# Kernel optimization log

Measured on AMD Instinct MI355X. Metric: run time of the kernel, lower is better.

## Reference

```python
import jax, jax.numpy as jnp
import numpy as np

B, S, E, H, NL = 64, 256, 1024, 16, 2
D = E // H          # head dim = 64
FF = 4 * E          # 4096
EPS = 1e-5
MASKED = -10000.0   # masked_bias buffer value


def layer_norm(x, g, b):
    m = jnp.mean(x, axis=-1, keepdims=True)
    v = jnp.mean(jnp.square(x - m), axis=-1, keepdims=True)
    return (x - m) * jax.lax.rsqrt(v + EPS) * g + b


def setup_inputs() -> dict:
    key = jax.random.key(0)
    ks = jax.random.split(key, 8)
    s = 0.02
    return {
        "sentence_hidden": jax.random.normal(ks[0], (B, S, E), dtype=jnp.float32),
        "wpe": jax.random.normal(ks[1], (256, E), dtype=jnp.float32) * s,
        "ln1_g": jnp.ones((NL, E), jnp.float32),
        "ln1_b": jnp.zeros((NL, E), jnp.float32),
        "attn_w": jax.random.normal(ks[2], (NL, E, 3 * E), dtype=jnp.float32) * s,
        "attn_b": jnp.zeros((NL, 3 * E), jnp.float32),
        "attn_proj_w": jax.random.normal(ks[3], (NL, E, E), dtype=jnp.float32) * s,
        "attn_proj_b": jnp.zeros((NL, E), jnp.float32),
        "ln2_g": jnp.ones((NL, E), jnp.float32),
        "ln2_b": jnp.zeros((NL, E), jnp.float32),
        "fc_w": jax.random.normal(ks[4], (NL, E, FF), dtype=jnp.float32) * s,
        "fc_b": jnp.zeros((NL, FF), jnp.float32),
        "mlp_proj_w": jax.random.normal(ks[5], (NL, FF, E), dtype=jnp.float32) * s,
        "mlp_proj_b": jnp.zeros((NL, E), jnp.float32),
        "lnf_g": jnp.ones((E,), jnp.float32),
        "lnf_b": jnp.zeros((E,), jnp.float32),
    }


def reference(sentence_hidden, wpe, ln1_g, ln1_b, attn_w, attn_b, attn_proj_w,
              attn_proj_b, ln2_g, ln2_b, fc_w, fc_b, mlp_proj_w, mlp_proj_b,
              lnf_g, lnf_b):
    # position embeddings: positions 0..S-1 (wpe has 256 rows, S == 256)
    h = sentence_hidden + wpe[:S][None, :, :]
    causal = jnp.tril(jnp.ones((S, S), dtype=bool))  # [S,S]
    scale = 1.0 / np.sqrt(D)
    for i in range(NL):
        # --- attention ---
        x = layer_norm(h, ln1_g[i], ln1_b[i])
        qkv = x @ attn_w[i] + attn_b[i]                    # [B,S,3E]
        q, k, v = jnp.split(qkv, 3, axis=-1)
        q = q.reshape(B, S, H, D).transpose(0, 2, 1, 3)    # [B,H,S,D]
        k = k.reshape(B, S, H, D).transpose(0, 2, 1, 3)
        v = v.reshape(B, S, H, D).transpose(0, 2, 1, 3)
        w = jnp.einsum("bhqd,bhkd->bhqk", q, k) * scale    # [B,H,S,S]
        w = jnp.where(causal, w, jnp.asarray(MASKED, w.dtype))
        w = jax.nn.softmax(w, axis=-1)
        a = jnp.einsum("bhqk,bhkd->bhqd", w, v)            # [B,H,S,D]
        a = a.transpose(0, 2, 1, 3).reshape(B, S, E)
        a = a @ attn_proj_w[i] + attn_proj_b[i]
        h = h + a
        # --- MLP ---
        x = layer_norm(h, ln2_g[i], ln2_b[i])
        m = jax.nn.gelu(x @ fc_w[i] + fc_b[i], approximate=True)  # gelu_new
        m = m @ mlp_proj_w[i] + mlp_proj_b[i]
        h = h + m
    h = layer_norm(h, lnf_g, lnf_b)
    loss = jnp.mean(jnp.square(h[0, :-1, :] - sentence_hidden[0, 1:, :]))
    return (h, loss)
```

## Files before the change

kernel.cpp:

```cpp
#include <hip/hip_runtime.h>
#include <cstdint>
#include <cstddef>


typedef __attribute__((ext_vector_type(4))) float f32x4;
typedef __attribute__((ext_vector_type(16))) float f32x16;
typedef __attribute__((ext_vector_type(8))) __bf16 bf16x8;
typedef __attribute__((ext_vector_type(4))) unsigned int u32x4;
typedef __attribute__((ext_vector_type(8))) unsigned short u16x8;
typedef __attribute__((ext_vector_type(4))) unsigned short u16x4;

__device__ __forceinline__ unsigned short f2bf(float x) {
  unsigned int u = __builtin_bit_cast(unsigned int, x);
  u += 0x7fffu + ((u >> 16) & 1u);
  return (unsigned short)(u >> 16);
}
__device__ __forceinline__ float gelu_new(float x) {
  float u = 0.7978845608028654f * (x + 0.044715f * x * x * x);
  return x * __builtin_amdgcn_rcpf(1.0f + __expf(-2.0f * u));
}
__device__ __forceinline__ unsigned int cvtpk(float lo, float hi) {
  unsigned int r;
  asm("v_cvt_pk_bf16_f32 %0, %1, %2" : "=v"(r) : "v"(lo), "v"(hi));
  return r;
}
__device__ __forceinline__ void plswap(unsigned int& a, unsigned int& b) {
  asm("v_permlane32_swap_b32 %0, %1" : "+v"(a), "+v"(b));
}

__global__ __launch_bounds__(256) void transpose_bf16(
    const float* __restrict__ W, unsigned short* __restrict__ Wt, int K, int N) {
  __shared__ float tile[32][33];
  const int n0 = blockIdx.x * 32, k0 = blockIdx.y * 32;
  const int tx = threadIdx.x, ty = threadIdx.y;
#pragma unroll
  for (int j = 0; j < 32; j += 8)
    tile[ty + j][tx] = W[(size_t)(k0 + ty + j) * N + n0 + tx];
  __syncthreads();
#pragma unroll
  for (int j = 0; j < 32; j += 8)
    Wt[(size_t)(n0 + ty + j) * K + k0 + tx] = f2bf(tile[tx][ty + j]);
}

__device__ __forceinline__ void ln_core(
    f32x4 v, const float* g, const float* bb, int row, int t,
    int outf32, void* outp) {
  float s = v.x + v.y + v.z + v.w;
  float sq = v.x * v.x + v.y * v.y + v.z * v.z + v.w * v.w;
#pragma unroll
  for (int off = 32; off; off >>= 1) {
    s += __shfl_xor(s, off, 64);
    sq += __shfl_xor(sq, off, 64);
  }
  __shared__ float red[8];
  if ((t & 63) == 0) { red[t >> 6] = s; red[4 + (t >> 6)] = sq; }
  __syncthreads();
  s = red[0] + red[1] + red[2] + red[3];
  sq = red[4] + red[5] + red[6] + red[7];
  const float mean = s * (1.0f / 1024.0f);
  const float var = sq * (1.0f / 1024.0f) - mean * mean;
  const float rs = rsqrtf(var + 1e-5f);
  const f32x4 gv = ((const f32x4*)g)[t];
  const f32x4 bv = ((const f32x4*)bb)[t];
  float y0 = (v.x - mean) * rs * gv.x + bv.x;
  float y1 = (v.y - mean) * rs * gv.y + bv.y;
  float y2 = (v.z - mean) * rs * gv.z + bv.z;
  float y3 = (v.w - mean) * rs * gv.w + bv.w;
  if (outf32) {
    f32x4 o; o.x = y0; o.y = y1; o.z = y2; o.w = y3;
    ((f32x4*)outp)[(size_t)row * 256 + t] = o;
  } else {
    u16x4 pk;
    pk.x = f2bf(y0); pk.y = f2bf(y1); pk.z = f2bf(y2); pk.w = f2bf(y3);
    ((u16x4*)outp)[(size_t)row * 256 + t] = pk;
  }
}

template <int OUTF32>
__global__ __launch_bounds__(256) void ln_kernel(
    const float* __restrict__ hin, const float* __restrict__ g,
    const float* __restrict__ bb, void* __restrict__ outp) {
  const int row = blockIdx.x, t = threadIdx.x;
  const f32x4 v = ((const f32x4*)(hin + (size_t)row * 1024))[t];
  ln_core(v, g, bb, row, t, OUTF32, outp);
}

__global__ __launch_bounds__(256) void ln_wpe_kernel(
    const float* __restrict__ sent, const float* __restrict__ wpe,
    const float* __restrict__ g, const float* __restrict__ bb,
    float* __restrict__ h, unsigned short* __restrict__ xb) {
  const int row = blockIdx.x, t = threadIdx.x;
  const int s = row & 255;
  f32x4 a = ((const f32x4*)(sent + (size_t)row * 1024))[t];
  f32x4 w = ((const f32x4*)(wpe + (size_t)s * 1024))[t];
  f32x4 v = a + w;
  ((f32x4*)(h + (size_t)row * 1024))[t] = v;
  ln_core(v, g, bb, row, t, 0, xb);
}

template <int BM, int EPI>
__global__ __launch_bounds__(512, 2) void gemm8p(
    const unsigned short* __restrict__ A, const unsigned short* __restrict__ Bt,
    const float* __restrict__ bias, unsigned short* __restrict__ Cb,
    float* __restrict__ Hres, int N, int K, int gx, int gy) {
  constexpr int M_REP = BM / 32;
  constexpr int MH = M_REP / 2;
  constexpr int A_E = BM * 64;
  constexpr int BUF_E = A_E + 16384;
  __shared__ alignas(16) unsigned short smem[2 * BUF_E];

  const int nwg = gx * gy;
  const int dd = blockIdx.x;
  const int wrk = (dd & 7) * (nwg >> 3) + (dd >> 3);
  const int stripe = gy * 4;
  const int cg = wrk / stripe;
  const int rem = wrk - cg * stripe;
  const int by = rem >> 2;
  const int bx = cg * 4 + (rem & 3);
  const int row0 = by * BM, col0 = bx * 256;

  const int t = threadIdx.x;
  const int wid = t >> 6, l = t & 63;
  const int wm = wid >> 2, wn = wid & 3;
  const int fr = l & 15, q4 = l >> 4;

  const int cx0 = (q4 ^ (fr & 7)) * 8;
  const int cx1 = ((4 + q4) ^ (fr & 7)) * 8;
  const int b_r0 = (wn * 64 + fr) * 64;
  auto a_slot = [&](int m) -> int {
    if constexpr (BM == 256) return (wm * 128 + m * 16 + fr) * 64;
    else return ((m >> 1) * 64 + wm * 32 + (m & 1) * 16 + fr) * 64;
  };

  const int lrow = l >> 3;
  const int scol = ((l & 7) ^ (lrow & 7)) * 8;

  auto stB = [&](int tt, int win) {
    const unsigned short* s =
        Bt + (size_t)(col0 + win * 8 + lrow) * K + tt * 64 + scol;
    __builtin_amdgcn_global_load_lds(
        (const __attribute__((address_space(1))) void*)s,
        (__attribute__((address_space(3))) void*)(smem + (tt & 1) * BUF_E + A_E + win * 512),
        16, 0, 0);
  };
  auto stA = [&](int tt, int win) {
    int rb;
    if constexpr (BM == 256) rb = win * 8;
    else rb = ((win >> 2) & 1) * 64 + (win >> 3) * 32 + (win & 3) * 8;
    const unsigned short* s =
        A + (size_t)(row0 + rb + lrow) * K + tt * 64 + scol;
    __builtin_amdgcn_global_load_lds(
        (const __attribute__((address_space(1))) void*)s,
        (__attribute__((address_space(3))) void*)(smem + (tt & 1) * BUF_E + win * 512),
        16, 0, 0);
  };
  auto stageB_set = [&](int tt) {
    stB(tt, 2 * wid); stB(tt, 2 * wid + 1);
    stB(tt, 16 + 2 * wid); stB(tt, 16 + 2 * wid + 1);
  };
  auto stageA_set = [&](int tt) {
    if constexpr (BM == 256) {
      const int i0 = 2 * wid, i1 = 2 * wid + 1;
      stA(tt, i0 < 8 ? i0 : 8 + i0);
      stA(tt, i1 < 8 ? i1 : 8 + i1);
      stA(tt, i0 < 8 ? 8 + i0 : 16 + i0);
      stA(tt, i1 < 8 ? 8 + i1 : 16 + i1);
    } else {
      stA(tt, wid);
      stA(tt, 8 + wid);
    }
  };
  constexpr int VM_BOUND = (BM == 256) ? 2 : 1;

  const int nt = K >> 6;

  stageB_set(0);
  stageA_set(0);
  asm volatile("s_waitcnt vmcnt(%0)" :: "i"(VM_BOUND) : "memory");
  __builtin_amdgcn_s_barrier();
  asm volatile("" ::: "memory");

  f32x4 acc[M_REP][4];
#pragma unroll
  for (int m = 0; m < M_REP; ++m)
#pragma unroll
    for (int n = 0; n < 4; ++n) {
      acc[m][n].x = 0.f; acc[m][n].y = 0.f; acc[m][n].z = 0.f; acc[m][n].w = 0.f;
    }

  for (int tc = 0; tc < nt; ++tc) {
    const unsigned short* Ab = smem + (tc & 1) * BUF_E;
    const unsigned short* Bb = Ab + A_E;
    const bool pf = (tc + 1) < nt;

    bf16x8 bfr[4][2], af[MH][2];
#pragma unroll
    for (int n = 0; n < 4; ++n) {
      bfr[n][0] = *(const bf16x8*)(Bb + b_r0 + n * 1024 + cx0);
      bfr[n][1] = *(const bf16x8*)(Bb + b_r0 + n * 1024 + cx1);
    }
#pragma unroll
    for (int m = 0; m < MH; ++m) {
      af[m][0] = *(const bf16x8*)(Ab + a_slot(m) + cx0);
      af[m][1] = *(const bf16x8*)(Ab + a_slot(m) + cx1);
    }
    if (pf) stageB_set(tc + 1);
    __builtin_amdgcn_s_setprio(1);
#pragma unroll
    for (int m = 0; m < MH; ++m)
#pragma unroll
      for (int n = 0; n < 4; ++n) {
        acc[m][n] = __builtin_amdgcn_mfma_f32_16x16x32_bf16(
            af[m][0], bfr[n][0], acc[m][n], 0, 0, 0);
        acc[m][n] = __builtin_amdgcn_mfma_f32_16x16x32_bf16(
            af[m][1], bfr[n][1], acc[m][n], 0, 0, 0);
      }
    __builtin_amdgcn_s_setprio(0);
    if (pf) asm volatile("s_waitcnt vmcnt(4)" ::: "memory");
    else    asm volatile("s_waitcnt vmcnt(0)" ::: "memory");
    __builtin_amdgcn_s_barrier();
    asm volatile("" ::: "memory");

    bf16x8 ah[MH][2];
#pragma unroll
    for (int m = 0; m < MH; ++m) {
      ah[m][0] = *(const bf16x8*)(Ab + a_slot(MH + m) + cx0);
      ah[m][1] = *(const bf16x8*)(Ab + a_slot(MH + m) + cx1);
    }
    if (pf) stageA_set(tc + 1);
    __builtin_amdgcn_s_setprio(1);
#pragma unroll
    for (int m = 0; m < MH; ++m)
#pragma unroll
      for (int n = 0; n < 4; ++n) {
        acc[MH + m][n] = __builtin_amdgcn_mfma_f32_16x16x32_bf16(
            ah[m][0], bfr[n][0], acc[MH + m][n], 0, 0, 0);
        acc[MH + m][n] = __builtin_amdgcn_mfma_f32_16x16x32_bf16(
            ah[m][1], bfr[n][1], acc[MH + m][n], 0, 0, 0);
      }
    __builtin_amdgcn_s_setprio(0);
    if (pf) asm volatile("s_waitcnt vmcnt(%0)" :: "i"(VM_BOUND) : "memory");
    else    asm volatile("s_waitcnt vmcnt(0)" ::: "memory");
    __builtin_amdgcn_s_barrier();
    asm volatile("" ::: "memory");
  }

  if constexpr (EPI == 2) {
#pragma unroll
    for (int n = 0; n < 4; ++n) {
      const int col = col0 + wn * 64 + n * 16 + fr;
      const float bi = bias[col];
#pragma unroll
      for (int m = 0; m < M_REP; ++m)
#pragma unroll
        for (int e = 0; e < 4; ++e) {
          const int row = row0 + wm * (BM / 2) + m * 16 + q4 * 4 + e;
          Hres[(size_t)row * N + col] += acc[m][n][e] + bi;
        }
    }
  } else {
    char* wreg = (char*)smem + wid * 9216;
    float bi[4];
#pragma unroll
    for (int n = 0; n < 4; ++n) bi[n] = bias[col0 + wn * 64 + n * 16 + fr];
#pragma unroll
    for (int half = 0; half < M_REP / 4; ++half) {
#pragma unroll
      for (int m = 0; m < 4; ++m)
#pragma unroll
        for (int n = 0; n < 4; ++n)
#pragma unroll
          for (int e = 0; e < 4; ++e) {
            float v = acc[half * 4 + m][n][e] + bi[n];
            if (EPI == 1) v = gelu_new(v);
            *(unsigned short*)(wreg + (m * 16 + q4 * 4 + e) * 144 +
                               (n * 16 + fr) * 2) = f2bf(v);
          }
#pragma unroll
      for (int rb = 0; rb < 8; ++rb) {
        const int rowl = rb * 8 + (l >> 3);
        u16x8 vv = *(const u16x8*)(wreg + rowl * 144 + (l & 7) * 16);
        const int rg = row0 + wm * (BM / 2) + half * 64 + rowl;
        *(u16x8*)(Cb + (size_t)rg * N + col0 + wn * 64 + (l & 7) * 8) = vv;
      }
    }
  }
}

__global__ __launch_bounds__(256) void attn_mfma(
    const unsigned short* __restrict__ qkv, unsigned short* __restrict__ aout,
    int b0) {
  __shared__ alignas(16) unsigned short Klds[256 * 64];
  __shared__ alignas(16) unsigned short Vt[64 * 256];
  const int bh = blockIdx.x;
  const int bl = bh >> 4, hd = bh & 15;
  const size_t base = (size_t)bl * 256 * 3072 + (size_t)hd * 64;
  const int t = threadIdx.x;
  const int w = t >> 6, l = t & 63;
  const int lq = l & 31, hl = l >> 5;

#pragma unroll
  for (int i = 0; i < 8; ++i) {
    const int r = i * 32 + (t >> 3);
    const int c = t & 7;
    u16x8 kv = *(const u16x8*)(qkv + base + (size_t)r * 3072 + 1024 + c * 8);
    *(u16x8*)(Klds + r * 64 + ((c ^ (r & 7)) * 8)) = kv;
    u16x8 vv = *(const u16x8*)(qkv + base + (size_t)r * 3072 + 2048 + c * 8);
#pragma unroll
    for (int j = 0; j < 8; ++j) {
      const int d = c * 8 + j;
      Vt[d * 256 + (((r >> 3) ^ (d & 31)) * 8) + (r & 7)] = vv[j];
    }
  }

  const int q0 = w * 64;
  bf16x8 qf[2][4];
#pragma unroll
  for (int n = 0; n < 2; ++n)
#pragma unroll
    for (int d16 = 0; d16 < 4; ++d16)
      qf[n][d16] = *(const bf16x8*)(qkv + base +
          (size_t)(q0 + n * 32 + lq) * 3072 + d16 * 16 + hl * 8);
  __syncthreads();

  const float cs = 0.125f * 1.44269504088896f;
  f32x16 O[2][2];
#pragma unroll
  for (int m = 0; m < 2; ++m)
#pragma unroll
    for (int n = 0; n < 2; ++n)
#pragma unroll
      for (int e = 0; e < 16; ++e) O[m][n][e] = 0.f;
  float mrun[2] = {-3.0e38f, -3.0e38f};
  float lrun[2] = {0.f, 0.f};

  const int ktmax = (q0 + 63) >> 5;
  for (int kt = 0; kt <= ktmax; ++kt) {
    bf16x8 kf[4];
    const int krow = kt * 32 + lq;
#pragma unroll
    for (int d16 = 0; d16 < 4; ++d16) {
      const int chunk = (d16 * 2 + hl) ^ (krow & 7);
      kf[d16] = *(const bf16x8*)(Klds + krow * 64 + chunk * 8);
    }
    const int nlo = (kt * 32 > q0 + 31) ? 1 : 0;
    bf16x8 pfrag[2][2];
#pragma unroll
    for (int n = 0; n < 2; ++n) {
      if (n < nlo) continue;
      f32x16 s;
#pragma unroll
      for (int e = 0; e < 16; ++e) s[e] = 0.f;
#pragma unroll
      for (int d16 = 0; d16 < 4; ++d16)
        s = __builtin_amdgcn_mfma_f32_32x32x16_bf16(kf[d16], qf[n][d16], s, 0, 0, 0);
      const int qg = q0 + n * 32 + lq;
      float sv[16];
#pragma unroll
      for (int r = 0; r < 16; ++r) {
        const int kg = kt * 32 + (r & 3) + 8 * (r >> 2) + 4 * hl;
        const float x = s[r] * cs;
        sv[r] = (kg > qg) ? -3.0e38f : x;
      }
      float pmax = sv[0];
#pragma unroll
      for (int r = 1; r < 16; ++r) pmax = fmaxf(pmax, sv[r]);
      pmax = fmaxf(pmax, __shfl_xor(pmax, 32, 64));
      const float nm = fmaxf(mrun[n], pmax);
      const float alpha = exp2f(mrun[n] - nm);
      mrun[n] = nm;
      float psum = 0.f;
#pragma unroll
      for (int r = 0; r < 16; ++r) {
        sv[r] = exp2f(sv[r] - nm);
        psum += sv[r];
      }
      psum += __shfl_xor(psum, 32, 64);
      lrun[n] = lrun[n] * alpha + psum;
#pragma unroll
      for (int m = 0; m < 2; ++m)
#pragma unroll
        for (int e = 0; e < 16; ++e) O[m][n][e] *= alpha;
#pragma unroll
      for (int h = 0; h < 2; ++h) {
        unsigned int a0 = cvtpk(sv[h * 8 + 0], sv[h * 8 + 1]);
        unsigned int a1 = cvtpk(sv[h * 8 + 2], sv[h * 8 + 3]);
        unsigned int c0 = cvtpk(sv[h * 8 + 4], sv[h * 8 + 5]);
        unsigned int c1 = cvtpk(sv[h * 8 + 6], sv[h * 8 + 7]);
        plswap(a0, c0);
        plswap(a1, c1);
        u32x4 fw; fw.x = a0; fw.y = a1; fw.z = c0; fw.w = c1;
        pfrag[n][h] = __builtin_bit_cast(bf16x8, fw);
      }
    }
#pragma unroll
    for (int m = 0; m < 2; ++m)
#pragma unroll
      for (int h = 0; h < 2; ++h) {
        const int dd = m * 32 + lq;
        const int chunk = (kt * 4 + h * 2 + hl) ^ (dd & 31);
        bf16x8 vf = *(const bf16x8*)(Vt + dd * 256 + chunk * 8);
#pragma unroll
        for (int n = 0; n < 2; ++n)
          if (n >= nlo)
            O[m][n] = __builtin_amdgcn_mfma_f32_32x32x16_bf16(vf, pfrag[n][h], O[m][n], 0, 0, 0);
      }
  }

#pragma unroll
  for (int n = 0; n < 2; ++n) {
    const float inv = 1.0f / lrun[n];
    const size_t row = (size_t)(b0 + bl) * 256 + q0 + n * 32 + lq;
#pragma unroll
    for (int m = 0; m < 2; ++m) {
#pragma unroll
      for (int qd = 0; qd < 4; ++qd) {
        u16x4 pk;
#pragma unroll
        for (int e = 0; e < 4; ++e) pk[e] = f2bf(O[m][n][qd * 4 + e] * inv);
        *(u16x4*)(aout + row * 1024 + hd * 64 + m * 32 + qd * 8 + hl * 4) = pk;
      }
    }
  }
}

__device__ __forceinline__ float block_reduce_sum256(float v) {
#pragma unroll
  for (int off = 32; off; off >>= 1) v += __shfl_xor(v, off, 64);
  __shared__ float red[4];
  const int t = threadIdx.x;
  if ((t & 63) == 0) red[t >> 6] = v;
  __syncthreads();
  return red[0] + red[1] + red[2] + red[3];
}

__global__ __launch_bounds__(256) void loss_partial(
    const float* __restrict__ hf, const float* __restrict__ sent,
    float* __restrict__ part) {
  const int s = blockIdx.x, t = threadIdx.x;
  f32x4 a = ((const f32x4*)(hf + (size_t)s * 1024))[t];
  f32x4 b = ((const f32x4*)(sent + (size_t)(s + 1) * 1024))[t];
  f32x4 d = a - b;
  float v = d.x * d.x + d.y * d.y + d.z * d.z + d.w * d.w;
  float tot = block_reduce_sum256(v);
  if (t == 0) part[s] = tot;
}

__global__ __launch_bounds__(256) void loss_final(
    const float* __restrict__ part, float* __restrict__ out) {
  const int t = threadIdx.x;
  float v = (t < 255) ? part[t] : 0.f;
  float s = block_reduce_sum256(v);
  if (t == 0) out[0] = s * (1.0f / (255.0f * 1024.0f));
}

constexpr size_t OFF_X     = 0;
constexpr size_t OFF_QKV   = 33554432;
constexpr size_t OFF_WQKV  = OFF_QKV + 67108864;
constexpr size_t OFF_WPROJ = OFF_WQKV + 6291456;
constexpr size_t OFF_WFC   = OFF_WPROJ + 2097152;
constexpr size_t OFF_WMLP  = OFF_WFC + 8388608;
constexpr size_t OFF_PART  = OFF_WMLP + 8388608;

extern "C" void kernel_launch(void* const* d_in, const int* in_sizes, int n_in,
                              void* d_out, int out_size, void* d_ws, size_t ws_size,
                              hipStream_t stream) {
  (void)in_sizes; (void)n_in; (void)out_size; (void)ws_size;
  const float* sent    = (const float*)d_in[0];
  const float* wpe     = (const float*)d_in[1];
  const float* ln1_g   = (const float*)d_in[2];
  const float* ln1_b   = (const float*)d_in[3];
  const float* attn_w  = (const float*)d_in[4];
  const float* attn_b  = (const float*)d_in[5];
  const float* attn_pw = (const float*)d_in[6];
  const float* attn_pb = (const float*)d_in[7];
  const float* ln2_g   = (const float*)d_in[8];
  const float* ln2_b   = (const float*)d_in[9];
  const float* fc_w    = (const float*)d_in[10];
  const float* fc_b    = (const float*)d_in[11];
  const float* mlp_w   = (const float*)d_in[12];
  const float* mlp_b   = (const float*)d_in[13];
  const float* lnf_g   = (const float*)d_in[14];
  const float* lnf_b   = (const float*)d_in[15];
  float* out_h = (float*)d_out;

  char* ws = (char*)d_ws;
  float* h              = out_h;
  unsigned short* xb    = (unsigned short*)(ws + OFF_X);
  unsigned short* qkvb  = (unsigned short*)(ws + OFF_QKV);
  unsigned short* mb    = (unsigned short*)(ws + OFF_QKV);
  unsigned short* wqkv  = (unsigned short*)(ws + OFF_WQKV);
  unsigned short* wproj = (unsigned short*)(ws + OFF_WPROJ);
  unsigned short* wfc   = (unsigned short*)(ws + OFF_WFC);
  unsigned short* wmlp  = (unsigned short*)(ws + OFF_WMLP);
  float* part           = (float*)(ws + OFF_PART);

  const dim3 tb(32, 8, 1);
  for (int i = 0; i < 2; ++i) {
    transpose_bf16<<<dim3(96, 32), tb, 0, stream>>>(
        attn_w + (size_t)i * 1024 * 3072, wqkv, 1024, 3072);
    transpose_bf16<<<dim3(32, 32), tb, 0, stream>>>(
        attn_pw + (size_t)i * 1024 * 1024, wproj, 1024, 1024);
    transpose_bf16<<<dim3(128, 32), tb, 0, stream>>>(
        fc_w + (size_t)i * 1024 * 4096, wfc, 1024, 4096);
    transpose_bf16<<<dim3(32, 128), tb, 0, stream>>>(
        mlp_w + (size_t)i * 4096 * 1024, wmlp, 4096, 1024);

    if (i == 0)
      ln_wpe_kernel<<<16384, 256, 0, stream>>>(sent, wpe, ln1_g, ln1_b, h, xb);
    else
      ln_kernel<0><<<16384, 256, 0, stream>>>(h, ln1_g + i * 1024, ln1_b + i * 1024, xb);
    for (int c = 0; c < 2; ++c) {
      const size_t r0 = (size_t)c * 8192;
      gemm8p<256, 0><<<384, 512, 0, stream>>>(
          xb + r0 * 1024, wqkv, attn_b + i * 3072, qkvb, nullptr, 3072, 1024, 12, 32);
      attn_mfma<<<512, 256, 0, stream>>>(qkvb, xb, c * 32);
    }
    gemm8p<256, 2><<<256, 512, 0, stream>>>(
        xb, wproj, attn_pb + i * 1024, nullptr, h, 1024, 1024, 4, 64);

    ln_kernel<0><<<16384, 256, 0, stream>>>(h, ln2_g + i * 1024, ln2_b + i * 1024, xb);
    for (int c = 0; c < 2; ++c) {
      const size_t r0 = (size_t)c * 8192;
      gemm8p<256, 1><<<512, 512, 0, stream>>>(
          xb + r0 * 1024, wfc, fc_b + i * 4096, mb, nullptr, 4096, 1024, 16, 32);
      gemm8p<128, 2><<<256, 512, 0, stream>>>(
          mb, wmlp, mlp_b + i * 1024, nullptr, h + r0 * 1024, 1024, 4096, 4, 64);
    }
  }

  ln_kernel<1><<<16384, 256, 0, stream>>>(h, lnf_g, lnf_b, out_h);
  loss_partial<<<255, 256, 0, stream>>>(out_h, sent, part);
  loss_final<<<1, 256, 0, stream>>>(part, out_h + 16777216);
}
```

Measured before the change: 1.257 ms.

## Add 4-phase 256x256 GEMM and process all rows at once when workspace allows

Adds a new gemm4p kernel that splits each K-step into four half-tile MFMA phases. Loads for the next tile are staged into LDS between phases, and MFMA sections run at raised wave priority. When the workspace is large enough, the QKV, attention and FC/MLP GEMMs run over the full 16384 rows in one launch instead of two 8192-row chunks, which raises the grid size and cuts launches. The path depends on ws_size, and the finer barrier scheduling could add sync overhead.

```diff
diff --git a/kernel.cpp b/kernel.cpp
--- a/kernel.cpp
+++ b/kernel.cpp
@@ -98,6 +98,197 @@
   ln_core(v, g, bb, row, t, 0, xb);
 }
 
+template <int EPI>
+__global__ __launch_bounds__(512, 2) void gemm4p(
+    const unsigned short* __restrict__ A, const unsigned short* __restrict__ Bt,
+    const float* __restrict__ bias, unsigned short* __restrict__ Cb,
+    float* __restrict__ Hres, int N, int K, int gx, int gy) {
+  constexpr int A_E = 16384;
+  constexpr int BUF_E = A_E + 16384;
+  __shared__ alignas(16) unsigned short smem[2 * BUF_E];
+
+  const int nwg = gx * gy;
+  const int dd = blockIdx.x;
+  const int wrk = (dd & 7) * (nwg >> 3) + (dd >> 3);
+  const int stripe = gy * 4;
+  const int cg = wrk / stripe;
+  const int rem = wrk - cg * stripe;
+  const int by = rem >> 2;
+  const int bx = cg * 4 + (rem & 3);
+  const int row0 = by * 256, col0 = bx * 256;
+
+  const int t = threadIdx.x;
+  const int wid = t >> 6, l = t & 63;
+  const int wm = wid >> 2, wn = wid & 3;
+  const int fr = l & 15, q4 = l >> 4;
+
+  const int cx0 = (q4 ^ (fr & 7)) * 8;
+  const int cx1 = ((4 + q4) ^ (fr & 7)) * 8;
+  const int b_r0 = (wn * 64 + fr) * 64;
+  auto a_slot = [&](int m) -> int { return (wm * 128 + m * 16 + fr) * 64; };
+
+  const int lrow = l >> 3;
+  const int scol = ((l & 7) ^ (lrow & 7)) * 8;
+
+  auto stB = [&](int tt, int win) {
+    const unsigned short* s =
+        Bt + (size_t)(col0 + win * 8 + lrow) * K + tt * 64 + scol;
+    __builtin_amdgcn_global_load_lds(
+        (const __attribute__((address_space(1))) void*)s,
+        (__attribute__((address_space(3))) void*)(smem + (tt & 1) * BUF_E + A_E + win * 512),
+        16, 0, 0);
+  };
+  auto stA = [&](int tt, int win) {
+    const unsigned short* s =
+        A + (size_t)(row0 + win * 8 + lrow) * K + tt * 64 + scol;
+    __builtin_amdgcn_global_load_lds(
+        (const __attribute__((address_space(1))) void*)s,
+        (__attribute__((address_space(3))) void*)(smem + (tt & 1) * BUF_E + win * 512),
+        16, 0, 0);
+  };
+  auto stageB_set = [&](int tt) {
+    stB(tt, 2 * wid); stB(tt, 2 * wid + 1);
+    stB(tt, 16 + 2 * wid); stB(tt, 16 + 2 * wid + 1);
+  };
+  auto stageA_set = [&](int tt) {
+    const int i0 = 2 * wid, i1 = 2 * wid + 1;
+    stA(tt, i0 < 8 ? i0 : 8 + i0);
+    stA(tt, i1 < 8 ? i1 : 8 + i1);
+    stA(tt, i0 < 8 ? 8 + i0 : 16 + i0);
+    stA(tt, i1 < 8 ? 8 + i1 : 16 + i1);
+  };
+
+  const int nt = K >> 6;
+
+  stageB_set(0);
+  stageA_set(0);
+  asm volatile("s_waitcnt vmcnt(2)" ::: "memory");
+  __builtin_amdgcn_s_barrier();
+  asm volatile("" ::: "memory");
+
+  f32x4 acc[8][4];
+#pragma unroll
+  for (int m = 0; m < 8; ++m)
+#pragma unroll
+    for (int n = 0; n < 4; ++n) {
+      acc[m][n].x = 0.f; acc[m][n].y = 0.f; acc[m][n].z = 0.f; acc[m][n].w = 0.f;
+    }
+
+  for (int tc = 0; tc < nt; ++tc) {
+    const unsigned short* Ab = smem + (tc & 1) * BUF_E;
+    const unsigned short* Bb = Ab + A_E;
+    const bool pf = (tc + 1) < nt;
+    bf16x8 bfr[4], af[4];
+
+#pragma unroll
+    for (int n = 0; n < 4; ++n) bfr[n] = *(const bf16x8*)(Bb + b_r0 + n * 1024 + cx0);
+#pragma unroll
+    for (int m = 0; m < 4; ++m) af[m] = *(const bf16x8*)(Ab + a_slot(m) + cx0);
+    if (pf) stageB_set(tc + 1);
+    __builtin_amdgcn_s_barrier();
+    asm volatile("" ::: "memory");
+    __builtin_amdgcn_s_setprio(1);
+#pragma unroll
+    for (int m = 0; m < 4; ++m)
+#pragma unroll
+      for (int n = 0; n < 4; ++n)
+        acc[m][n] = __builtin_amdgcn_mfma_f32_16x16x32_bf16(af[m], bfr[n], acc[m][n], 0, 0, 0);
+    __builtin_amdgcn_s_setprio(0);
+    if (pf) asm volatile("s_waitcnt vmcnt(4)" ::: "memory");
+    else    asm volatile("s_waitcnt vmcnt(0)" ::: "memory");
+    __builtin_amdgcn_s_barrier();
+    asm volatile("" ::: "memory");
+
+#pragma unroll
+    for (int m = 0; m < 4; ++m) af[m] = *(const bf16x8*)(Ab + a_slot(4 + m) + cx0);
+    if (pf) stageA_set(tc + 1);
+    __builtin_amdgcn_s_barrier();
+    asm volatile("" ::: "memory");
+    __builtin_amdgcn_s_setprio(1);
+#pragma unroll
+    for (int m = 0; m < 4; ++m)
+#pragma unroll
+      for (int n = 0; n < 4; ++n)
+        acc[4 + m][n] = __builtin_amdgcn_mfma_f32_16x16x32_bf16(af[m], bfr[n], acc[4 + m][n], 0, 0, 0);
+    __builtin_amdgcn_s_setprio(0);
+    __builtin_amdgcn_s_barrier();
+    asm volatile("" ::: "memory");
+
+#pragma unroll
+    for (int n = 0; n < 4; ++n) bfr[n] = *(const bf16x8*)(Bb + b_r0 + n * 1024 + cx1);
+#pragma unroll
+    for (int m = 0; m < 4; ++m) af[m] = *(const bf16x8*)(Ab + a_slot(m) + cx1);
+    __builtin_amdgcn_s_barrier();
+    asm volatile("" ::: "memory");
+    __builtin_amdgcn_s_setprio(1);
+#pragma unroll
+    for (int m = 0; m < 4; ++m)
+#pragma unroll
+      for (int n = 0; n < 4; ++n)
+        acc[m][n] = __builtin_amdgcn_mfma_f32_16x16x32_bf16(af[m], bfr[n], acc[m][n], 0, 0, 0);
+    __builtin_amdgcn_s_setprio(0);
+    __builtin_amdgcn_s_barrier();
+    asm volatile("" ::: "memory");
+
+#pragma unroll
+    for (int m = 0; m < 4; ++m) af[m] = *(const bf16x8*)(Ab + a_slot(4 + m) + cx1);
+    __builtin_amdgcn_s_barrier();
+    asm volatile("" ::: "memory");
+    __builtin_amdgcn_s_setprio(1);
+#pragma unroll
+    for (int m = 0; m < 4; ++m)
+#pragma unroll
+      for (int n = 0; n < 4; ++n)
+        acc[4 + m][n] = __builtin_amdgcn_mfma_f32_16x16x32_bf16(af[m], bfr[n], acc[4 + m][n], 0, 0, 0);
+    __builtin_amdgcn_s_setprio(0);
+    if (pf) asm volatile("s_waitcnt vmcnt(2)" ::: "memory");
+    else    asm volatile("s_waitcnt vmcnt(0)" ::: "memory");
+    __builtin_amdgcn_s_barrier();
+    asm volatile("" ::: "memory");
+  }
+
+  if constexpr (EPI == 2) {
+#pragma unroll
+    for (int n = 0; n < 4; ++n) {
+      const int col = col0 + wn * 64 + n * 16 + fr;
+      const float bi = bias[col];
+#pragma unroll
+      for (int m = 0; m < 8; ++m)
+#pragma unroll
+        for (int e = 0; e < 4; ++e) {
+          const int row = row0 + wm * 128 + m * 16 + q4 * 4 + e;
+          Hres[(size_t)row * N + col] += acc[m][n][e] + bi;
+        }
+    }
+  } else {
+    char* wreg = (char*)smem + wid * 9216;
+    float bi[4];
+#pragma unroll
+    for (int n = 0; n < 4; ++n) bi[n] = bias[col0 + wn * 64 + n * 16 + fr];
+#pragma unroll
+    for (int half = 0; half < 2; ++half) {
+#pragma unroll
+      for (int m = 0; m < 4; ++m)
+#pragma unroll
+        for (int n = 0; n < 4; ++n)
+#pragma unroll
+          for (int e = 0; e < 4; ++e) {
+            float v = acc[half * 4 + m][n][e] + bi[n];
+            if (EPI == 1) v = gelu_new(v);
+            *(unsigned short*)(wreg + (m * 16 + q4 * 4 + e) * 144 +
+                               (n * 16 + fr) * 2) = f2bf(v);
+          }
+#pragma unroll
+      for (int rb = 0; rb < 8; ++rb) {
+        const int rowl = rb * 8 + (l >> 3);
+        u16x8 vv = *(const u16x8*)(wreg + rowl * 144 + (l & 7) * 16);
+        const int rg = row0 + wm * 128 + half * 64 + rowl;
+        *(u16x8*)(Cb + (size_t)rg * N + col0 + wn * 64 + (l & 7) * 8) = vv;
+      }
+    }
+  }
+}
+
 template <int BM, int EPI>
 __global__ __launch_bounds__(512, 2) void gemm8p(
     const unsigned short* __restrict__ A, const unsigned short* __restrict__ Bt,
@@ -454,18 +645,27 @@
   if (t == 0) out[0] = s * (1.0f / (255.0f * 1024.0f));
 }
 
-constexpr size_t OFF_X     = 0;
-constexpr size_t OFF_QKV   = 33554432;
-constexpr size_t OFF_WQKV  = OFF_QKV + 67108864;
-constexpr size_t OFF_WPROJ = OFF_WQKV + 6291456;
-constexpr size_t OFF_WFC   = OFF_WPROJ + 2097152;
-constexpr size_t OFF_WMLP  = OFF_WFC + 8388608;
-constexpr size_t OFF_PART  = OFF_WMLP + 8388608;
+constexpr size_t C_X     = 0;
+constexpr size_t C_QKV   = 33554432;
+constexpr size_t C_WQKV  = C_QKV + 67108864;
+constexpr size_t C_WPROJ = C_WQKV + 6291456;
+constexpr size_t C_WFC   = C_WPROJ + 2097152;
+constexpr size_t C_WMLP  = C_WFC + 8388608;
+constexpr size_t C_PART  = C_WMLP + 8388608;
+
+constexpr size_t F_X     = 0;
+constexpr size_t F_U     = 33554432;
+constexpr size_t F_WQKV  = F_U + 134217728;
+constexpr size_t F_WPROJ = F_WQKV + 6291456;
+constexpr size_t F_WFC   = F_WPROJ + 2097152;
+constexpr size_t F_WMLP  = F_WFC + 8388608;
+constexpr size_t F_PART  = F_WMLP + 8388608;
+constexpr size_t F_NEED  = F_PART + 4096;
 
 extern "C" void kernel_launch(void* const* d_in, const int* in_sizes, int n_in,
                               void* d_out, int out_size, void* d_ws, size_t ws_size,
                               hipStream_t stream) {
-  (void)in_sizes; (void)n_in; (void)out_size; (void)ws_size;
+  (void)in_sizes; (void)n_in; (void)out_size;
   const float* sent    = (const float*)d_in[0];
   const float* wpe     = (const float*)d_in[1];
   const float* ln1_g   = (const float*)d_in[2];
@@ -483,17 +683,18 @@
   const float* lnf_g   = (const float*)d_in[14];
   const float* lnf_b   = (const float*)d_in[15];
   float* out_h = (float*)d_out;
+  float* h = out_h;
 
   char* ws = (char*)d_ws;
-  float* h              = out_h;
-  unsigned short* xb    = (unsigned short*)(ws + OFF_X);
-  unsigned short* qkvb  = (unsigned short*)(ws + OFF_QKV);
-  unsigned short* mb    = (unsigned short*)(ws + OFF_QKV);
-  unsigned short* wqkv  = (unsigned short*)(ws + OFF_WQKV);
-  unsigned short* wproj = (unsigned short*)(ws + OFF_WPROJ);
-  unsigned short* wfc   = (unsigned short*)(ws + OFF_WFC);
-  unsigned short* wmlp  = (unsigned short*)(ws + OFF_WMLP);
-  float* part           = (float*)(ws + OFF_PART);
+  const bool fullm = ws_size >= F_NEED;
+
+  unsigned short* xb    = (unsigned short*)(ws + (fullm ? F_X : C_X));
+  unsigned short* ub    = (unsigned short*)(ws + (fullm ? F_U : C_QKV));
+  unsigned short* wqkv  = (unsigned short*)(ws + (fullm ? F_WQKV : C_WQKV));
+  unsigned short* wproj = (unsigned short*)(ws + (fullm ? F_WPROJ : C_WPROJ));
+  unsigned short* wfc   = (unsigned short*)(ws + (fullm ? F_WFC : C_WFC));
+  unsigned short* wmlp  = (unsigned short*)(ws + (fullm ? F_WMLP : C_WMLP));
+  float* part           = (float*)(ws + (fullm ? F_PART : C_PART));
 
   const dim3 tb(32, 8, 1);
   for (int i = 0; i < 2; ++i) {
@@ -510,22 +711,36 @@
       ln_wpe_kernel<<<16384, 256, 0, stream>>>(sent, wpe, ln1_g, ln1_b, h, xb);
     else
       ln_kernel<0><<<16384, 256, 0, stream>>>(h, ln1_g + i * 1024, ln1_b + i * 1024, xb);
-    for (int c = 0; c < 2; ++c) {
-      const size_t r0 = (size_t)c * 8192;
-      gemm8p<256, 0><<<384, 512, 0, stream>>>(
-          xb + r0 * 1024, wqkv, attn_b + i * 3072, qkvb, nullptr, 3072, 1024, 12, 32);
-      attn_mfma<<<512, 256, 0, stream>>>(qkvb, xb, c * 32);
-    }
-    gemm8p<256, 2><<<256, 512, 0, stream>>>(
+
+    if (fullm) {
+      gemm4p<0><<<768, 512, 0, stream>>>(
+          xb, wqkv, attn_b + i * 3072, ub, nullptr, 3072, 1024, 12, 64);
+      attn_mfma<<<1024, 256, 0, stream>>>(ub, xb, 0);
+    } else {
+      for (int c = 0; c < 2; ++c) {
+        const size_t r0 = (size_t)c * 8192;
+        gemm4p<0><<<384, 512, 0, stream>>>(
+            xb + r0 * 1024, wqkv, attn_b + i * 3072, ub, nullptr, 3072, 1024, 12, 32);
+        attn_mfma<<<512, 256, 0, stream>>>(ub, xb, c * 32);
+      }
+    }
+    gemm4p<2><<<256, 512, 0, stream>>>(
         xb, wproj, attn_pb + i * 1024, nullptr, h, 1024, 1024, 4, 64);
 
     ln_kernel<0><<<16384, 256, 0, stream>>>(h, ln2_g + i * 1024, ln2_b + i * 1024, xb);
-    for (int c = 0; c < 2; ++c) {
-      const size_t r0 = (size_t)c * 8192;
-      gemm8p<256, 1><<<512, 512, 0, stream>>>(
-          xb + r0 * 1024, wfc, fc_b + i * 4096, mb, nullptr, 4096, 1024, 16, 32);
-      gemm8p<128, 2><<<256, 512, 0, stream>>>(
-          mb, wmlp, mlp_b + i * 1024, nullptr, h + r0 * 1024, 1024, 4096, 4, 64);
+    if (fullm) {
+      gemm4p<1><<<1024, 512, 0, stream>>>(
+          xb, wfc, fc_b + i * 4096, ub, nullptr, 4096, 1024, 16, 64);
+      gemm4p<2><<<256, 512, 0, stream>>>(
+          ub, wmlp, mlp_b + i * 1024, nullptr, h, 1024, 4096, 4, 64);
+    } else {
+      for (int c = 0; c < 2; ++c) {
+        const size_t r0 = (size_t)c * 8192;
+        gemm4p<1><<<512, 512, 0, stream>>>(
+            xb + r0 * 1024, wfc, fc_b + i * 4096, ub, nullptr, 4096, 1024, 16, 32);
+        gemm8p<128, 2><<<256, 512, 0, stream>>>(
+            ub, wmlp, mlp_b + i * 1024, nullptr, h + r0 * 1024, 1024, 4096, 4, 64);
+      }
     }
   }
 
```

Result: faster. 1.189 ms (-5.4%).

## Process full batch in single GEMM launches when workspace allows; unify 256-row tiles

Applied to the files above, without the earlier changes.

When the workspace is large enough, the QKV, attention, FC and MLP-projection stages each run as one launch over all 16384 rows instead of two half-batch chunks. The separate BM=128 GEMM variant is removed, so the MLP down-projection now also uses 256x256 tiles. The k-loop is reordered to load and issue MFMAs per 32-wide k-half, with A prefetch interleaved between them, and block rasterization is changed to group along rows. This cuts launch count and improves wave fill, but the larger intermediate buffer needs more workspace and the MLP-down grid shrinks to 128 blocks per chunk in the fallback path.

```diff
diff --git a/kernel.cpp b/kernel.cpp
--- a/kernel.cpp
+++ b/kernel.cpp
@@ -98,26 +98,23 @@
   ln_core(v, g, bb, row, t, 0, xb);
 }
 
-template <int BM, int EPI>
-__global__ __launch_bounds__(512, 2) void gemm8p(
+template <int EPI>
+__global__ __launch_bounds__(512, 2) void gemmp(
     const unsigned short* __restrict__ A, const unsigned short* __restrict__ Bt,
     const float* __restrict__ bias, unsigned short* __restrict__ Cb,
     float* __restrict__ Hres, int N, int K, int gx, int gy) {
-  constexpr int M_REP = BM / 32;
-  constexpr int MH = M_REP / 2;
-  constexpr int A_E = BM * 64;
+  constexpr int A_E = 16384;
   constexpr int BUF_E = A_E + 16384;
   __shared__ alignas(16) unsigned short smem[2 * BUF_E];
 
   const int nwg = gx * gy;
   const int dd = blockIdx.x;
   const int wrk = (dd & 7) * (nwg >> 3) + (dd >> 3);
-  const int stripe = gy * 4;
-  const int cg = wrk / stripe;
-  const int rem = wrk - cg * stripe;
-  const int by = rem >> 2;
-  const int bx = cg * 4 + (rem & 3);
-  const int row0 = by * BM, col0 = bx * 256;
+  const int grp = wrk / (gx * 4);
+  const int r = wrk - grp * (gx * 4);
+  const int bx = r >> 2;
+  const int by = grp * 4 + (r & 3);
+  const int row0 = by * 256, col0 = bx * 256;
 
   const int t = threadIdx.x;
   const int wid = t >> 6, l = t & 63;
@@ -127,10 +124,7 @@
   const int cx0 = (q4 ^ (fr & 7)) * 8;
   const int cx1 = ((4 + q4) ^ (fr & 7)) * 8;
   const int b_r0 = (wn * 64 + fr) * 64;
-  auto a_slot = [&](int m) -> int {
-    if constexpr (BM == 256) return (wm * 128 + m * 16 + fr) * 64;
-    else return ((m >> 1) * 64 + wm * 32 + (m & 1) * 16 + fr) * 64;
-  };
+  auto a_slot = [&](int m) -> int { return (wm * 128 + m * 16 + fr) * 64; };
 
   const int lrow = l >> 3;
   const int scol = ((l & 7) ^ (lrow & 7)) * 8;
@@ -144,11 +138,8 @@
         16, 0, 0);
   };
   auto stA = [&](int tt, int win) {
-    int rb;
-    if constexpr (BM == 256) rb = win * 8;
-    else rb = ((win >> 2) & 1) * 64 + (win >> 3) * 32 + (win & 3) * 8;
     const unsigned short* s =
-        A + (size_t)(row0 + rb + lrow) * K + tt * 64 + scol;
+        A + (size_t)(row0 + win * 8 + lrow) * K + tt * 64 + scol;
     __builtin_amdgcn_global_load_lds(
         (const __attribute__((address_space(1))) void*)s,
         (__attribute__((address_space(3))) void*)(smem + (tt & 1) * BUF_E + win * 512),
@@ -159,30 +150,24 @@
     stB(tt, 16 + 2 * wid); stB(tt, 16 + 2 * wid + 1);
   };
   auto stageA_set = [&](int tt) {
-    if constexpr (BM == 256) {
-      const int i0 = 2 * wid, i1 = 2 * wid + 1;
-      stA(tt, i0 < 8 ? i0 : 8 + i0);
-      stA(tt, i1 < 8 ? i1 : 8 + i1);
-      stA(tt, i0 < 8 ? 8 + i0 : 16 + i0);
-      stA(tt, i1 < 8 ? 8 + i1 : 16 + i1);
-    } else {
-      stA(tt, wid);
-      stA(tt, 8 + wid);
-    }
+    const int i0 = 2 * wid, i1 = 2 * wid + 1;
+    stA(tt, i0 < 8 ? i0 : 8 + i0);
+    stA(tt, i1 < 8 ? i1 : 8 + i1);
+    stA(tt, i0 < 8 ? 8 + i0 : 16 + i0);
+    stA(tt, i1 < 8 ? 8 + i1 : 16 + i1);
   };
-  constexpr int VM_BOUND = (BM == 256) ? 2 : 1;
 
   const int nt = K >> 6;
 
   stageB_set(0);
   stageA_set(0);
-  asm volatile("s_waitcnt vmcnt(%0)" :: "i"(VM_BOUND) : "memory");
+  asm volatile("s_waitcnt vmcnt(2)" ::: "memory");
   __builtin_amdgcn_s_barrier();
   asm volatile("" ::: "memory");
 
-  f32x4 acc[M_REP][4];
-#pragma unroll
-  for (int m = 0; m < M_REP; ++m)
+  f32x4 acc[8][4];
+#pragma unroll
+  for (int m = 0; m < 8; ++m)
 #pragma unroll
     for (int n = 0; n < 4; ++n) {
       acc[m][n].x = 0.f; acc[m][n].y = 0.f; acc[m][n].z = 0.f; acc[m][n].w = 0.f;
@@ -193,53 +178,63 @@
     const unsigned short* Bb = Ab + A_E;
     const bool pf = (tc + 1) < nt;
 
-    bf16x8 bfr[4][2], af[MH][2];
-#pragma unroll
-    for (int n = 0; n < 4; ++n) {
-      bfr[n][0] = *(const bf16x8*)(Bb + b_r0 + n * 1024 + cx0);
-      bfr[n][1] = *(const bf16x8*)(Bb + b_r0 + n * 1024 + cx1);
-    }
-#pragma unroll
-    for (int m = 0; m < MH; ++m) {
-      af[m][0] = *(const bf16x8*)(Ab + a_slot(m) + cx0);
-      af[m][1] = *(const bf16x8*)(Ab + a_slot(m) + cx1);
-    }
+    bf16x8 b0[4], b1[4], a0[4], a1[4];
+#pragma unroll
+    for (int n = 0; n < 4; ++n) b0[n] = *(const bf16x8*)(Bb + b_r0 + n * 1024 + cx0);
+#pragma unroll
+    for (int m = 0; m < 4; ++m) a0[m] = *(const bf16x8*)(Ab + a_slot(m) + cx0);
+#pragma unroll
+    for (int n = 0; n < 4; ++n) b1[n] = *(const bf16x8*)(Bb + b_r0 + n * 1024 + cx1);
+#pragma unroll
+    for (int m = 0; m < 4; ++m) a1[m] = *(const bf16x8*)(Ab + a_slot(m) + cx1);
+
     if (pf) stageB_set(tc + 1);
+
     __builtin_amdgcn_s_setprio(1);
 #pragma unroll
-    for (int m = 0; m < MH; ++m)
-#pragma unroll
-      for (int n = 0; n < 4; ++n) {
-        acc[m][n] = __builtin_amdgcn_mfma_f32_16x16x32_bf16(
-            af[m][0], bfr[n][0], acc[m][n], 0, 0, 0);
-        acc[m][n] = __builtin_amdgcn_mfma_f32_16x16x32_bf16(
-            af[m][1], bfr[n][1], acc[m][n], 0, 0, 0);
-      }
+    for (int m = 0; m < 4; ++m)
+#pragma unroll
+      for (int n = 0; n < 4; ++n)
+        acc[m][n] = __builtin_amdgcn_mfma_f32_16x16x32_bf16(a0[m], b0[n], acc[m][n], 0, 0, 0);
     __builtin_amdgcn_s_setprio(0);
-    if (pf) asm volatile("s_waitcnt vmcnt(4)" ::: "memory");
+
+    if (pf) stageA_set(tc + 1);
+
+    __builtin_amdgcn_s_setprio(1);
+#pragma unroll
+    for (int m = 0; m < 4; ++m)
+#pragma unroll
+      for (int n = 0; n < 4; ++n)
+        acc[m][n] = __builtin_amdgcn_mfma_f32_16x16x32_bf16(a1[m], b1[n], acc[m][n], 0, 0, 0);
+    __builtin_amdgcn_s_setprio(0);
+
+    if (pf) asm volatile("s_waitcnt vmcnt(8)" ::: "memory");
     else    asm volatile("s_waitcnt vmcnt(0)" ::: "memory");
     __builtin_amdgcn_s_barrier();
     asm volatile("" ::: "memory");
 
-    bf16x8 ah[MH][2];
-#pragma unroll
-    for (int m = 0; m < MH; ++m) {
-      ah[m][0] = *(const bf16x8*)(Ab + a_slot(MH + m) + cx0);
-      ah[m][1] = *(const bf16x8*)(Ab + a_slot(MH + m) + cx1);
-    }
-    if (pf) stageA_set(tc + 1);
+    bf16x8 h0[4], h1[4];
+#pragma unroll
+    for (int m = 0; m < 4; ++m) h0[m] = *(const bf16x8*)(Ab + a_slot(4 + m) + cx0);
+#pragma unroll
+    for (int m = 0; m < 4; ++m) h1[m] = *(const bf16x8*)(Ab + a_slot(4 + m) + cx1);
+
     __builtin_amdgcn_s_setprio(1);
 #pragma unroll
-    for (int m = 0; m < MH; ++m)
-#pragma unroll
-      for (int n = 0; n < 4; ++n) {
-        acc[MH + m][n] = __builtin_amdgcn_mfma_f32_16x16x32_bf16(
-            ah[m][0], bfr[n][0], acc[MH + m][n], 0, 0, 0);
-        acc[MH + m][n] = __builtin_amdgcn_mfma_f32_16x16x32_bf16(
-            ah[m][1], bfr[n][1], acc[MH + m][n], 0, 0, 0);
-      }
+    for (int m = 0; m < 4; ++m)
+#pragma unroll
+      for (int n = 0; n < 4; ++n)
+        acc[4 + m][n] = __builtin_amdgcn_mfma_f32_16x16x32_bf16(h0[m], b0[n], acc[4 + m][n], 0, 0, 0);
     __builtin_amdgcn_s_setprio(0);
-    if (pf) asm volatile("s_waitcnt vmcnt(%0)" :: "i"(VM_BOUND) : "memory");
+    __builtin_amdgcn_s_setprio(1);
+#pragma unroll
+    for (int m = 0; m < 4; ++m)
+#pragma unroll
+      for (int n = 0; n < 4; ++n)
+        acc[4 + m][n] = __builtin_amdgcn_mfma_f32_16x16x32_bf16(h1[m], b1[n], acc[4 + m][n], 0, 0, 0);
+    __builtin_amdgcn_s_setprio(0);
+
+    if (pf) asm volatile("s_waitcnt vmcnt(2)" ::: "memory");
     else    asm volatile("s_waitcnt vmcnt(0)" ::: "memory");
     __builtin_amdgcn_s_barrier();
     asm volatile("" ::: "memory");
@@ -251,10 +246,10 @@
       const int col = col0 + wn * 64 + n * 16 + fr;
       const float bi = bias[col];
 #pragma unroll
-      for (int m = 0; m < M_REP; ++m)
+      for (int m = 0; m < 8; ++m)
 #pragma unroll
         for (int e = 0; e < 4; ++e) {
-          const int row = row0 + wm * (BM / 2) + m * 16 + q4 * 4 + e;
+          const int row = row0 + wm * 128 + m * 16 + q4 * 4 + e;
           Hres[(size_t)row * N + col] += acc[m][n][e] + bi;
         }
     }
@@ -264,7 +259,7 @@
 #pragma unroll
     for (int n = 0; n < 4; ++n) bi[n] = bias[col0 + wn * 64 + n * 16 + fr];
 #pragma unroll
-    for (int half = 0; half < M_REP / 4; ++half) {
+    for (int half = 0; half < 2; ++half) {
 #pragma unroll
       for (int m = 0; m < 4; ++m)
 #pragma unroll
@@ -280,7 +275,7 @@
       for (int rb = 0; rb < 8; ++rb) {
         const int rowl = rb * 8 + (l >> 3);
         u16x8 vv = *(const u16x8*)(wreg + rowl * 144 + (l & 7) * 16);
-        const int rg = row0 + wm * (BM / 2) + half * 64 + rowl;
+        const int rg = row0 + wm * 128 + half * 64 + rowl;
         *(u16x8*)(Cb + (size_t)rg * N + col0 + wn * 64 + (l & 7) * 8) = vv;
       }
     }
@@ -454,18 +449,27 @@
   if (t == 0) out[0] = s * (1.0f / (255.0f * 1024.0f));
 }
 
-constexpr size_t OFF_X     = 0;
-constexpr size_t OFF_QKV   = 33554432;
-constexpr size_t OFF_WQKV  = OFF_QKV + 67108864;
-constexpr size_t OFF_WPROJ = OFF_WQKV + 6291456;
-constexpr size_t OFF_WFC   = OFF_WPROJ + 2097152;
-constexpr size_t OFF_WMLP  = OFF_WFC + 8388608;
-constexpr size_t OFF_PART  = OFF_WMLP + 8388608;
+constexpr size_t C_X     = 0;
+constexpr size_t C_QKV   = 33554432;
+constexpr size_t C_WQKV  = C_QKV + 67108864;
+constexpr size_t C_WPROJ = C_WQKV + 6291456;
+constexpr size_t C_WFC   = C_WPROJ + 2097152;
+constexpr size_t C_WMLP  = C_WFC + 8388608;
+constexpr size_t C_PART  = C_WMLP + 8388608;
+
+constexpr size_t F_X     = 0;
+constexpr size_t F_U     = 33554432;
+constexpr size_t F_WQKV  = F_U + 134217728;
+constexpr size_t F_WPROJ = F_WQKV + 6291456;
+constexpr size_t F_WFC   = F_WPROJ + 2097152;
+constexpr size_t F_WMLP  = F_WFC + 8388608;
+constexpr size_t F_PART  = F_WMLP + 8388608;
+constexpr size_t F_NEED  = F_PART + 4096;
 
 extern "C" void kernel_launch(void* const* d_in, const int* in_sizes, int n_in,
                               void* d_out, int out_size, void* d_ws, size_t ws_size,
                               hipStream_t stream) {
-  (void)in_sizes; (void)n_in; (void)out_size; (void)ws_size;
+  (void)in_sizes; (void)n_in; (void)out_size;
   const float* sent    = (const float*)d_in[0];
   const float* wpe     = (const float*)d_in[1];
   const float* ln1_g   = (const float*)d_in[2];
@@ -483,17 +487,18 @@
   const float* lnf_g   = (const float*)d_in[14];
   const float* lnf_b   = (const float*)d_in[15];
   float* out_h = (float*)d_out;
+  float* h = out_h;
 
   char* ws = (char*)d_ws;
-  float* h              = out_h;
-  unsigned short* xb    = (unsigned short*)(ws + OFF_X);
-  unsigned short* qkvb  = (unsigned short*)(ws + OFF_QKV);
-  unsigned short* mb    = (unsigned short*)(ws + OFF_QKV);
-  unsigned short* wqkv  = (unsigned short*)(ws + OFF_WQKV);
-  unsigned short* wproj = (unsigned short*)(ws + OFF_WPROJ);
-  unsigned short* wfc   = (unsigned short*)(ws + OFF_WFC);
-  unsigned short* wmlp  = (unsigned short*)(ws + OFF_WMLP);
-  float* part           = (float*)(ws + OFF_PART);
+  const bool fullm = ws_size >= F_NEED;
+
+  unsigned short* xb    = (unsigned short*)(ws + (fullm ? F_X : C_X));
+  unsigned short* ub    = (unsigned short*)(ws + (fullm ? F_U : C_QKV));
+  unsigned short* wqkv  = (unsigned short*)(ws + (fullm ? F_WQKV : C_WQKV));
+  unsigned short* wproj = (unsigned short*)(ws + (fullm ? F_WPROJ : C_WPROJ));
+  unsigned short* wfc   = (unsigned short*)(ws + (fullm ? F_WFC : C_WFC));
+  unsigned short* wmlp  = (unsigned short*)(ws + (fullm ? F_WMLP : C_WMLP));
+  float* part           = (float*)(ws + (fullm ? F_PART : C_PART));
 
   const dim3 tb(32, 8, 1);
   for (int i = 0; i < 2; ++i) {
@@ -510,22 +515,36 @@
       ln_wpe_kernel<<<16384, 256, 0, stream>>>(sent, wpe, ln1_g, ln1_b, h, xb);
     else
       ln_kernel<0><<<16384, 256, 0, stream>>>(h, ln1_g + i * 1024, ln1_b + i * 1024, xb);
-    for (int c = 0; c < 2; ++c) {
-      const size_t r0 = (size_t)c * 8192;
-      gemm8p<256, 0><<<384, 512, 0, stream>>>(
-          xb + r0 * 1024, wqkv, attn_b + i * 3072, qkvb, nullptr, 3072, 1024, 12, 32);
-      attn_mfma<<<512, 256, 0, stream>>>(qkvb, xb, c * 32);
-    }
-    gemm8p<256, 2><<<256, 512, 0, stream>>>(
+
+    if (fullm) {
+      gemmp<0><<<768, 512, 0, stream>>>(
+          xb, wqkv, attn_b + i * 3072, ub, nullptr, 3072, 1024, 12, 64);
+      attn_mfma<<<1024, 256, 0, stream>>>(ub, xb, 0);
+    } else {
+      for (int c = 0; c < 2; ++c) {
+        const size_t r0 = (size_t)c * 8192;
+        gemmp<0><<<384, 512, 0, stream>>>(
+            xb + r0 * 1024, wqkv, attn_b + i * 3072, ub, nullptr, 3072, 1024, 12, 32);
+        attn_mfma<<<512, 256, 0, stream>>>(ub, xb, c * 32);
+      }
+    }
+    gemmp<2><<<256, 512, 0, stream>>>(
         xb, wproj, attn_pb + i * 1024, nullptr, h, 1024, 1024, 4, 64);
 
     ln_kernel<0><<<16384, 256, 0, stream>>>(h, ln2_g + i * 1024, ln2_b + i * 1024, xb);
-    for (int c = 0; c < 2; ++c) {
-      const size_t r0 = (size_t)c * 8192;
-      gemm8p<256, 1><<<512, 512, 0, stream>>>(
-          xb + r0 * 1024, wfc, fc_b + i * 4096, mb, nullptr, 4096, 1024, 16, 32);
-      gemm8p<128, 2><<<256, 512, 0, stream>>>(
-          mb, wmlp, mlp_b + i * 1024, nullptr, h + r0 * 1024, 1024, 4096, 4, 64);
+    if (fullm) {
+      gemmp<1><<<1024, 512, 0, stream>>>(
+          xb, wfc, fc_b + i * 4096, ub, nullptr, 4096, 1024, 16, 64);
+      gemmp<2><<<256, 512, 0, stream>>>(
+          ub, wmlp, mlp_b + i * 1024, nullptr, h, 1024, 4096, 4, 64);
+    } else {
+      for (int c = 0; c < 2; ++c) {
+        const size_t r0 = (size_t)c * 8192;
+        gemmp<1><<<512, 512, 0, stream>>>(
+            xb + r0 * 1024, wfc, fc_b + i * 4096, ub, nullptr, 4096, 1024, 16, 32);
+        gemmp<2><<<128, 512, 0, stream>>>(
+            ub, wmlp, mlp_b + i * 1024, nullptr, h + r0 * 1024, 1024, 4096, 4, 32);
+      }
     }
   }
 
```

Result: faster. 1.138 ms (-9.5%).
